# Performance work log

Measured on AMD Instinct MI355X. Metric: run time of the kernel, lower is better.

Reference implementation:

```python
import jax, jax.numpy as jnp
import numpy as np

S_DIM = 4096
N_NODES = 4096
N_EDGES = 32768


def _coarsen(ei_np, N):
    """Integer-only greedy coarsening, faithful to MNGRAPH.forward's while-loop.
    Returns (select order, flattened neighbor indices, segment ids, per-hub
    neighbor counts, forward-fill indices replicating the stale-M behavior for
    empty neighborhoods, and the remapped final edge_index)."""
    ei = ei_np.astype(np.int64).copy()
    I = np.bincount(ei[0], minlength=N)
    O = np.bincount(ei[1], minlength=N)
    order = np.argsort(-(I + O), kind='stable')  # torch.argsort(D, descending=True)
    visits = np.zeros(N, dtype=bool)
    select = []
    nbr_idx, nbr_seg, counts = [], [], []
    while order.size > 0:
        node = int(order[0])
        select.append(node)
        visits[node] = True
        # H = unique neighbors of node in the CURRENT (rewritten) edge_index
        H = np.unique(np.concatenate([ei[1][ei[0] == node], ei[0][ei[1] == node]]))
        visits[H] = True
        order = order[~visits[order]]
        # rewrite: endpoints in H that are not already-selected hubs -> node
        Hn = H[~np.isin(H, np.asarray(select, dtype=np.int64))]
        ei[np.isin(ei, Hn)] = node
        ei = ei[:, ei[0] != ei[1]]  # drop self-loops
        # append reversed edges that are not already present (pair-code isin
        # == the original O(E^2) all/any comparison, computed efficiently)
        code = ei[0] * N + ei[1]
        rcode = ei[1] * N + ei[0]
        new = ~np.isin(rcode, code)
        ei = np.concatenate([ei, ei[::-1][:, new]], axis=1)
        k = len(select) - 1
        nbr_idx.append(H)
        nbr_seg.append(np.full(H.shape[0], k, dtype=np.int64))
        counts.append(H.shape[0])
    select = np.asarray(select, dtype=np.int64)
    sort_sel = np.sort(select)
    ei_out = np.searchsorted(sort_sel, ei)  # compact node ids
    counts = np.asarray(counts, dtype=np.int64)
    # forward-fill: when H is empty the original appends the previous (stale) M
    fill = np.arange(select.shape[0])
    for i in range(select.shape[0]):
        if counts[i] == 0:
            fill[i] = fill[i - 1] if i > 0 else 0
    nbr = np.concatenate(nbr_idx) if nbr_idx else np.zeros(0, np.int64)
    seg = np.concatenate(nbr_seg) if nbr_seg else np.zeros(0, np.int64)
    return select, nbr, seg, counts, fill, ei_out


def setup_inputs() -> dict:
    key = jax.random.key(0)
    k1, k2, k3, k4 = jax.random.split(key, 4)
    x = jax.random.normal(k1, (N_NODES, S_DIM), dtype=jnp.float32)
    edge_index = jax.random.randint(k2, (2, N_EDGES), 0, N_NODES, dtype=jnp.int64)
    bound = float(np.sqrt(6.0 / (1.0 + S_DIM)))  # xavier_uniform on (1, S)
    W1 = jax.random.uniform(k3, (S_DIM,), jnp.float32, -bound, bound)
    W2 = jax.random.uniform(k4, (S_DIM,), jnp.float32, -bound, bound)
    B1 = jnp.zeros((S_DIM,), jnp.float32)
    B2 = jnp.zeros((S_DIM,), jnp.float32)
    return {"x": x, "edge_index": edge_index, "W1": W1, "W2": W2, "B1": B1, "B2": B2}


def reference(x, edge_index, W1, W2, B1, B2):
    N = x.shape[0]
    sel, nbr, seg, counts, fill, ei_out = _coarsen(np.asarray(edge_index), N)
    K = sel.shape[0]
    # Dn = x[n]*W1+B1 for every neighbor of every hub; per-hub mean via segment_sum
    Dn = x[jnp.asarray(nbr)] * W1 + B1                      # [T, S]
    sums = jax.ops.segment_sum(Dn, jnp.asarray(seg), num_segments=K)
    denom = jnp.maximum(jnp.asarray(counts), 1).astype(x.dtype)[:, None]
    mean_Dn = sums / denom                                  # [K, S]
    Dv = x[jnp.asarray(sel)] * W2 + B2                      # [K, S]
    END = jnp.concatenate([Dv, mean_Dn], axis=1)            # [K, 2S]
    END = END[jnp.asarray(fill)]                            # stale-M replication
    return END, jnp.asarray(ei_out)
```

## Files before the change

kernel.cpp:

```cpp
#include <hip/hip_runtime.h>
#include <hip/hip_bf16.h>

#define NT 1024
#define NNODES 4096
#define ECAP 65536

__device__ __forceinline__ int blockScanExcl(int v, int* s_w, int* total) {
    const int tid  = threadIdx.x;
    const int lane = tid & 63;
    const int wv   = tid >> 6;
    int x = v;
#pragma unroll
    for (int off = 1; off < 64; off <<= 1) {
        int t = __shfl_up(x, off, 64);
        if (lane >= off) x += t;
    }
    if (lane == 63) s_w[wv] = x;
    __syncthreads();
    if (tid < 16) {
        int y = s_w[tid];
#pragma unroll
        for (int off = 1; off < 16; off <<= 1) {
            int t = __shfl_up(y, off, 16);
            if (tid >= off) y += t;
        }
        s_w[tid] = y;
    }
    __syncthreads();
    int base = wv ? s_w[wv - 1] : 0;
    int tot  = s_w[15];
    __syncthreads();
    *total = tot;
    return base + x - v;
}

__global__ __launch_bounds__(NT, 1)
void phaseA1(const int* __restrict__ ei, int E0,
             int* __restrict__ U, int* __restrict__ V,
             unsigned int* __restrict__ BM,
             int* __restrict__ NBR, int* __restrict__ OTH,
             int* __restrict__ ORDV, int* __restrict__ ROFFG, int* __restrict__ RENDG,
             int* __restrict__ HAND)
{
    __shared__ unsigned short s_order[NNODES];
    __shared__ unsigned char  s_vis[NNODES];
    __shared__ unsigned int   s_hb[NNODES / 32];
    __shared__ int s_roff[NNODES];
    __shared__ int s_rend[NNODES];
    __shared__ int s_tmp[NNODES];
    __shared__ int s_w[16];
    __shared__ int s_bc[16];

    const int tid = threadIdx.x;

    for (int i = tid; i < NNODES; i += NT) { s_vis[i] = 0; s_tmp[i] = 0; }
    for (int i = tid; i < NNODES / 32; i += NT) s_hb[i] = 0;
    if (tid < 16) s_bc[tid] = 0;
    __syncthreads();

    for (int i = tid; i < E0; i += NT)
        if (ei[2 * i + 1] != 0) s_bc[9] = 1;
    __syncthreads();
    const int is64 = !s_bc[9];

    for (int e = tid; e < E0; e += NT) {
        int uu = ei[is64 ? 2 * e : e];
        int vv = ei[is64 ? 2 * (E0 + e) : (E0 + e)];
        U[e] = uu; V[e] = vv;
        atomicAdd(&s_tmp[uu], 1);
        atomicAdd(&s_tmp[vv], 1);
    }
    __syncthreads();
    for (int n = tid; n < NNODES; n += NT) atomicMax(&s_bc[7], s_tmp[n]);
    __syncthreads();
    const int maxd = s_bc[7];

    for (int d = maxd; d >= 0; --d) {
        int n0 = tid * 4;
        int f0 = (s_tmp[n0] == d), f1 = (s_tmp[n0 + 1] == d);
        int f2 = (s_tmp[n0 + 2] == d), f3 = (s_tmp[n0 + 3] == d);
        int tot;
        int off = blockScanExcl(f0 + f1 + f2 + f3, s_w, &tot);
        int idx = s_bc[4] + off;
        if (f0) s_order[idx++] = (unsigned short)n0;
        if (f1) s_order[idx++] = (unsigned short)(n0 + 1);
        if (f2) s_order[idx++] = (unsigned short)(n0 + 2);
        if (f3) s_order[idx++] = (unsigned short)(n0 + 3);
        __syncthreads();
        if (tid == 0) s_bc[4] += tot;
        __syncthreads();
    }

    if (tid == 0) {
        int nd = s_order[0];
        s_bc[0] = nd; s_vis[nd] = 1;
    }
    __syncthreads();
    {
        const int node = s_bc[0];
        for (int e = tid; e < E0; e += NT) {
            int uu = U[e], vv = V[e];
            if (uu == node) {
                int w = vv; unsigned m = 1u << (w & 31);
                unsigned old = atomicOr(&s_hb[w >> 5], m);
                if (!(old & m)) { int i = atomicAdd(&s_bc[2], 1); s_tmp[i] = w; s_vis[w] = 1; }
            }
            if (vv == node) {
                int w = uu; unsigned m = 1u << (w & 31);
                unsigned old = atomicOr(&s_hb[w >> 5], m);
                if (!(old & m)) { int i = atomicAdd(&s_bc[2], 1); s_tmp[i] = w; s_vis[w] = 1; }
            }
        }
        __syncthreads();
        for (int e = tid; e < E0; e += NT) {
            int uu = U[e];
            if (uu != node && ((s_hb[uu >> 5] >> (uu & 31)) & 1)) U[e] = node;
            int vv = V[e];
            if (vv != node && ((s_hb[vv >> 5] >> (vv & 31)) & 1)) V[e] = node;
        }
        __syncthreads();
    }

    for (int i = tid; i < (1 << 19); i += NT) BM[i] = 0u;
    __syncthreads();
    for (int e = tid; e < E0; e += NT) {
        int uu = U[e], vv = V[e];
        if (uu != vv) {
            unsigned code = ((unsigned)uu << 12) | (unsigned)vv;
            atomicOr(&BM[code >> 5], 1u << (code & 31));
        }
    }
    __syncthreads();
    for (int t = 0; t < E0; t += NT) {
        int e = t + tid, flag = 0, uu = 0, vv = 0;
        if (e < E0) {
            uu = U[e]; vv = V[e];
            if (uu != vv) {
                unsigned rc = ((unsigned)vv << 12) | (unsigned)uu;
                unsigned old = atomicOr(&BM[rc >> 5], 0u);
                flag = !((old >> (rc & 31)) & 1u);
            }
        }
        int tot;
        int off = blockScanExcl(flag, s_w, &tot);
        if (flag) { int r = s_bc[5] + off; U[E0 + r] = vv; V[E0 + r] = uu; }
        __syncthreads();
        if (tid == 0) s_bc[5] += tot;
        __syncthreads();
    }
    const int E1 = E0 + s_bc[5];

    for (int n = tid; n < NNODES; n += NT) s_roff[n] = 0;
    __syncthreads();
    for (int e = tid; e < E1; e += NT) {
        int uu = U[e], vv = V[e];
        if (uu != vv) { atomicAdd(&s_roff[uu], 1); atomicAdd(&s_roff[vv], 1); }
    }
    __syncthreads();
    {
        int n0 = tid * 4;
        int c0 = s_roff[n0], c1 = s_roff[n0 + 1], c2 = s_roff[n0 + 2], c3 = s_roff[n0 + 3];
        int tot;
        int off = blockScanExcl(c0 + c1 + c2 + c3, s_w, &tot);
        int st = off;
        s_roff[n0] = st;     s_rend[n0] = st;     st += c0;
        s_roff[n0 + 1] = st; s_rend[n0 + 1] = st; st += c1;
        s_roff[n0 + 2] = st; s_rend[n0 + 2] = st; st += c2;
        s_roff[n0 + 3] = st; s_rend[n0 + 3] = st;
    }
    __syncthreads();
    for (int e = tid; e < E1; e += NT) {
        int uu = U[e], vv = V[e];
        if (uu != vv) {
            int p = atomicAdd(&s_rend[uu], 1);
            int q = atomicAdd(&s_rend[vv], 1);
            OTH[p] = vv; OTH[q] = uu;
        }
    }
    __syncthreads();
    {
        const int cnt0 = s_bc[2];
        for (int i = tid; i < cnt0; i += NT) NBR[i] = s_tmp[i];
    }
    for (int i = tid; i < NNODES; i += NT) {
        int nd = (int)s_order[i];
        ORDV[i]  = nd | (s_vis[nd] ? 0x8000 : 0);
        ROFFG[i] = s_roff[i];
        RENDG[i] = s_rend[i];
    }
    if (tid == 0) { HAND[0] = E1; HAND[1] = s_bc[2]; HAND[2] = s_bc[0]; }
}

__global__ __launch_bounds__(64, 1)
void phaseA2(const int* __restrict__ OTH, int* __restrict__ NBR,
             const int* __restrict__ ORDV, const int* __restrict__ ROFFG,
             const int* __restrict__ RENDG, const int* __restrict__ HAND,
             int* __restrict__ SEL, int* __restrict__ CNTS,
             int* __restrict__ NST, int* __restrict__ FIL, int* __restrict__ SC,
             int* __restrict__ LABG, int* __restrict__ RNKG)
{
    __shared__ unsigned short s_ordvis[NNODES];
    __shared__ unsigned short s_pos[NNODES];
    __shared__ unsigned short s_lab[NNODES];
    __shared__ unsigned short s_so[NNODES];
    __shared__ int s_cnt[NNODES];
    __shared__ int s_stamp[NNODES];
    __shared__ int s_roff[NNODES];
    __shared__ int s_rend[NNODES];
    __shared__ unsigned char s_sel[NNODES];
    __shared__ int s_nc[1];

    const int ln = threadIdx.x;
    const unsigned long long ltm = (1ull << ln) - 1ull;
    const int cnt0 = HAND[1], hub0 = HAND[2];

    for (int i = ln; i < NNODES; i += 64) {
        int ov = ORDV[i];
        s_ordvis[i] = (unsigned short)ov;
        s_pos[ov & 0x7FFF] = (unsigned short)i;
        s_roff[i] = ROFFG[i];
        s_rend[i] = RENDG[i];
        s_lab[i] = (unsigned short)i;
        s_stamp[i] = 0; s_sel[i] = 0; s_cnt[i] = 0;
    }
    if (ln == 0) {
        s_sel[hub0] = 1; s_so[0] = (unsigned short)hub0;
        s_cnt[0] = cnt0; s_nc[0] = cnt0;
    }

    int p = 0, k = 1;
    for (;;) {
        int node = -1;
        while (p < NNODES) {
            int idx = p + ln;
            int ov = (idx < NNODES) ? (int)s_ordvis[idx] : 0x8000;
            unsigned long long bal = __ballot(!(ov & 0x8000));
            if (bal != 0ull) {
                int sl = __ffsll((long long)bal) - 1;
                node = __shfl(ov, sl, 64) & 0x7FFF;
                p += sl + 1;
                break;
            }
            p += 64;
        }
        if (node < 0) break;
        if (ln == 0) { s_sel[node] = 1; s_so[k] = (unsigned short)node; }
        const int rb = s_roff[node], re = s_rend[node];
        const int begin = s_nc[0];
        for (int s0 = rb; s0 < re; s0 += 128) {
            int sA = s0 + ln, sB = s0 + 64 + ln;
            int oA = (sA < re) ? OTH[sA] : -1;
            int oB = (sB < re) ? OTH[sB] : -1;
            if (oA >= 0) {
                int w = (int)s_lab[oA];
                if (w != node) {
                    int old = atomicMax(&s_stamp[w], k);
                    if (old < k) {
                        int i = atomicAdd(&s_nc[0], 1);
                        NBR[i] = w;
                        s_ordvis[s_pos[w]] = (unsigned short)(0x8000 | w);
                        if (!s_sel[w]) s_lab[w] = (unsigned short)node;
                    }
                }
            }
            if (oB >= 0) {
                int w = (int)s_lab[oB];
                if (w != node) {
                    int old = atomicMax(&s_stamp[w], k);
                    if (old < k) {
                        int i = atomicAdd(&s_nc[0], 1);
                        NBR[i] = w;
                        s_ordvis[s_pos[w]] = (unsigned short)(0x8000 | w);
                        if (!s_sel[w]) s_lab[w] = (unsigned short)node;
                    }
                }
            }
        }
        if (ln == 0) s_cnt[k] = s_nc[0] - begin;
        k++;
    }
    const int K = k;

    {
        int base = 0;
        for (int c = 0; c < NNODES / 64; ++c) {
            int n = c * 64 + ln;
            int f = s_sel[n];
            unsigned long long b = __ballot(f);
            s_stamp[n] = base + __popcll(b & ltm);
            base += __popcll(b);
        }
    }
    {
        int nb = 0;
        for (int c = 0; c * 64 < K; ++c) {
            int i = c * 64 + ln;
            int cv = (i < K) ? s_cnt[i] : 0;
            int x = cv;
#pragma unroll
            for (int off = 1; off < 64; off <<= 1) {
                int t = __shfl_up(x, off, 64);
                if (ln >= off) x += t;
            }
            if (i < K) { NST[i] = nb + x - cv; CNTS[i] = cv; SEL[i] = (int)s_so[i]; }
            nb += __shfl(x, 63, 64);
        }
    }
    {
        int carry = 0;
        for (int c = 0; c * 64 < K; ++c) {
            int i = c * 64 + ln;
            int f = (i < K) && (s_cnt[i] > 0);
            unsigned long long b = __ballot(f);
            unsigned long long m = b & ((ln == 63) ? ~0ull : ((1ull << (ln + 1)) - 1ull));
            int fil = m ? (c * 64 + 63 - __clzll(m)) : carry;
            if (i < K) FIL[i] = fil;
            carry = b ? (c * 64 + 63 - __clzll(b)) : carry;
        }
    }
    if (ln == 0) SC[0] = K;
    for (int i = ln; i < NNODES; i += 64) {
        LABG[i] = (int)s_lab[i];
        RNKG[i] = s_stamp[i];
    }
}

__global__ __launch_bounds__(NT, 1)
void phaseA3(const int* __restrict__ U, const int* __restrict__ V,
             const int* __restrict__ LABG, const int* __restrict__ RNKG,
             const int* __restrict__ HAND, int* __restrict__ SC,
             int* __restrict__ TMP, float* __restrict__ out)
{
    __shared__ unsigned short l_lab[NNODES];
    __shared__ int l_rnk[NNODES];
    __shared__ int s_w[16];
    __shared__ int s_base[1];

    const int tid = threadIdx.x;
    for (int i = tid; i < NNODES; i += NT) {
        l_lab[i] = (unsigned short)LABG[i];
        l_rnk[i] = RNKG[i];
    }
    if (tid == 0) s_base[0] = 0;
    __syncthreads();

    const int E1 = HAND[0];
    const int K  = SC[0];
    const size_t obase = (size_t)K * 8192;

    for (int t = 0; t < E1; t += NT) {
        int e = t + tid, flag = 0, ru = 0, rv = 0;
        if (e < E1) {
            int uu = (int)l_lab[U[e]], vv = (int)l_lab[V[e]];
            if (uu != vv) { flag = 1; ru = l_rnk[uu]; rv = l_rnk[vv]; }
        }
        int tot;
        int off = blockScanExcl(flag, s_w, &tot);
        if (flag) {
            int r = s_base[0] + off;
            out[obase + (size_t)r] = (float)ru;
            TMP[r] = rv;
        }
        __syncthreads();
        if (tid == 0) s_base[0] += tot;
        __syncthreads();
    }
    const int Ef = s_base[0];
    if (tid == 0) SC[1] = Ef;
    for (int r = tid; r < Ef; r += NT)
        out[obase + (size_t)Ef + (size_t)r] = (float)TMP[r];
}

__global__ __launch_bounds__(256, 4)
void phaseB(const float* __restrict__ x,
            const float* __restrict__ W1, const float* __restrict__ W2,
            const float* __restrict__ B1, const float* __restrict__ B2,
            const int* __restrict__ NBR, const int* __restrict__ SEL,
            const int* __restrict__ CNTS, const int* __restrict__ NST,
            const int* __restrict__ FIL, const int* __restrict__ SC,
            float* __restrict__ out)
{
    const int K = SC[0];
    const int k = blockIdx.x;
    if (k >= K) return;
    const int kk   = FIL[k];
    const int node = SEL[kk];
    const int cnt  = CNTS[kk];
    const int st   = NST[kk];
    const int tid  = threadIdx.x;
    const float4* x4 = (const float4*)x;

    float4 acc[4];
#pragma unroll
    for (int j = 0; j < 4; j++) acc[j] = make_float4(0.f, 0.f, 0.f, 0.f);

    for (int r = 0; r < cnt; ++r) {
        const float4* row = x4 + (size_t)NBR[st + r] * 1024;
#pragma unroll
        for (int j = 0; j < 4; j++) {
            float4 t = row[tid + j * 256];
            acc[j].x += t.x; acc[j].y += t.y; acc[j].z += t.z; acc[j].w += t.w;
        }
    }

    const float fc  = (float)cnt;
    const float inv = 1.0f / (float)(cnt > 1 ? cnt : 1);
    const float4* xr = x4 + (size_t)node * 1024;
    float4* o4 = (float4*)(out + (size_t)k * 8192);

#pragma unroll
    for (int j = 0; j < 4; j++) {
        int c = tid + j * 256;
        float4 w1 = ((const float4*)W1)[c], b1 = ((const float4*)B1)[c];
        float4 w2 = ((const float4*)W2)[c], b2 = ((const float4*)B2)[c];
        float4 xv = xr[c];
        float4 pd, pm;
        pd.x = xv.x * w2.x + b2.x;
        pd.y = xv.y * w2.y + b2.y;
        pd.z = xv.z * w2.z + b2.z;
        pd.w = xv.w * w2.w + b2.w;
        pm.x = (acc[j].x * w1.x + fc * b1.x) * inv;
        pm.y = (acc[j].y * w1.y + fc * b1.y) * inv;
        pm.z = (acc[j].z * w1.z + fc * b1.z) * inv;
        pm.w = (acc[j].w * w1.w + fc * b1.w) * inv;
        o4[c] = pd;
        o4[1024 + c] = pm;
    }
}

extern "C" void kernel_launch(void* const* d_in, const int* in_sizes, int n_in,
                              void* d_out, int out_size, void* d_ws, size_t ws_size,
                              hipStream_t stream)
{
    const float* x  = (const float*)d_in[0];
    const int*   ei = (const int*)d_in[1];
    const float* W1 = (const float*)d_in[2];
    const float* W2 = (const float*)d_in[3];
    const float* B1 = (const float*)d_in[4];
    const float* B2 = (const float*)d_in[5];
    const int E0 = in_sizes[1] / 2;

    char* w = (char*)d_ws;
    int* U = (int*)w;
    int* V = U + ECAP;
    unsigned int* BM = (unsigned int*)(V + ECAP);
    int* OTH = (int*)BM;
    int* NBR = OTH + 2 * ECAP;
    int* TMP = NBR + 2 * ECAP;
    char* meta = (char*)BM + (2u << 20);
    int* SEL   = (int*)meta;
    int* CNTS  = SEL  + NNODES;
    int* NST   = CNTS + NNODES;
    int* FIL   = NST  + NNODES;
    int* SC    = FIL  + NNODES;
    int* ORDV  = SC   + 16;
    int* ROFFG = ORDV + NNODES;
    int* RENDG = ROFFG + NNODES;
    int* LABG  = RENDG + NNODES;
    int* RNKG  = LABG + NNODES;
    int* HAND  = RNKG + NNODES;
    float* out = (float*)d_out;

    hipLaunchKernelGGL(phaseA1, dim3(1), dim3(NT), 0, stream,
                       ei, E0, U, V, BM, NBR, OTH, ORDV, ROFFG, RENDG, HAND);
    hipLaunchKernelGGL(phaseA2, dim3(1), dim3(64), 0, stream,
                       OTH, NBR, ORDV, ROFFG, RENDG, HAND,
                       SEL, CNTS, NST, FIL, SC, LABG, RNKG);
    hipLaunchKernelGGL(phaseA3, dim3(1), dim3(NT), 0, stream,
                       U, V, LABG, RNKG, HAND, SC, TMP, out);
    hipLaunchKernelGGL(phaseB, dim3(NNODES), dim3(256), 0, stream,
                       x, W1, W2, B1, B2, NBR, SEL, CNTS, NST, FIL, SC, out);
}
```

Measured before the change: 965.9 us.

## Restructure coarsening phases: parallel degree sort, prefetching hub loop, chunked compaction

Replaces the per-degree scan loop that built the descending-degree order with a second block doing a counting sort using wave ballots, and picks the first hub with an atomicMin. The serial hub-selection loop in phaseA2 now prefetches the next candidate's adjacency while processing the current one, and uses ballot-based cursor allocation instead of shared atomics. Edge compaction in phaseA1 and phaseA3 uses per-thread chunk bitmasks with a single block scan in place of many scan-plus-sync rounds. phaseB is split over a second grid dimension to get more blocks. These target the long single-block serial latency chain, at the cost of more complex control flow and chunk masks that assume at most 64 edges per thread.

Result: slower. 1.179 ms (+22.1%).

```diff
diff --git a/kernel.cpp b/kernel.cpp
--- a/kernel.cpp
+++ b/kernel.cpp
@@ -39,10 +39,12 @@
              int* __restrict__ U, int* __restrict__ V,
              unsigned int* __restrict__ BM,
              int* __restrict__ NBR, int* __restrict__ OTH,
-             int* __restrict__ ORDV, int* __restrict__ ROFFG, int* __restrict__ RENDG,
-             int* __restrict__ HAND)
+             int* __restrict__ ORDG, int* __restrict__ ROFFG, int* __restrict__ RENDG,
+             int* __restrict__ STAMPG, int* __restrict__ HAND)
 {
-    __shared__ unsigned short s_order[NNODES];
+    __shared__ int t_deg[NNODES];
+    __shared__ int t_cur[NNODES];
+    __shared__ int t_bc[4];
     __shared__ unsigned char  s_vis[NNODES];
     __shared__ unsigned int   s_hb[NNODES / 32];
     __shared__ int s_roff[NNODES];
@@ -53,9 +55,66 @@
 
     const int tid = threadIdx.x;
 
+    if (blockIdx.x == 1) {
+        for (int i = tid; i < NNODES; i += NT) { t_deg[i] = 0; t_cur[i] = 0; }
+        if (tid < 4) t_bc[tid] = 0;
+        __syncthreads();
+        for (int i = tid; i < E0; i += NT)
+            if (ei[2 * i + 1] != 0) t_bc[1] = 1;
+        __syncthreads();
+        const int is64b = !t_bc[1];
+        for (int e = tid; e < E0; e += NT) {
+            int uu = ei[is64b ? 2 * e : e];
+            int vv = ei[is64b ? 2 * (E0 + e) : (E0 + e)];
+            atomicAdd(&t_deg[uu], 1);
+            atomicAdd(&t_deg[vv], 1);
+        }
+        __syncthreads();
+        for (int n = tid; n < NNODES; n += NT) atomicMax(&t_bc[2], t_deg[n]);
+        __syncthreads();
+        const int maxd = t_bc[2];
+        for (int n = tid; n < NNODES; n += NT) atomicAdd(&t_cur[t_deg[n]], 1);
+        __syncthreads();
+        if (tid < 64) {
+            const int ln = tid;
+            const unsigned long long ltm = (1ull << ln) - 1ull;
+            int carry = 0;
+            for (int b0 = 0; b0 <= maxd; b0 += 64) {
+                int d = b0 + ln;
+                int v = (d <= maxd) ? t_cur[d] : 0;
+                int x = v;
+#pragma unroll
+                for (int off = 1; off < 64; off <<= 1) {
+                    int t = __shfl_up(x, off, 64);
+                    if (ln >= off) x += t;
+                }
+                if (d <= maxd) t_cur[d] = NNODES - (carry + x);
+                carry += __shfl(x, 63, 64);
+            }
+            const int nb = 32 - __clz(maxd | 1);
+            for (int g = 0; g < NNODES / 64; ++g) {
+                int n = g * 64 + ln;
+                int d = t_deg[n];
+                unsigned long long m = ~0ull;
+                for (int b = 0; b < nb; ++b) {
+                    unsigned long long bb = __ballot((d >> b) & 1);
+                    m &= ((d >> b) & 1) ? bb : ~bb;
+                }
+                int rank   = __popcll(m & ltm);
+                int leader = __ffsll((long long)m) - 1;
+                int base = 0;
+                if (ln == leader) { base = t_cur[d]; t_cur[d] = base + __popcll(m); }
+                base = __shfl(base, leader, 64);
+                ORDG[base + rank] = n;
+            }
+        }
+        return;
+    }
+
     for (int i = tid; i < NNODES; i += NT) { s_vis[i] = 0; s_tmp[i] = 0; }
     for (int i = tid; i < NNODES / 32; i += NT) s_hb[i] = 0;
     if (tid < 16) s_bc[tid] = 0;
+    if (tid == 0) s_bc[0] = 0x7fffffff;
     __syncthreads();
 
     for (int i = tid; i < E0; i += NT)
@@ -74,27 +133,11 @@
     for (int n = tid; n < NNODES; n += NT) atomicMax(&s_bc[7], s_tmp[n]);
     __syncthreads();
     const int maxd = s_bc[7];
-
-    for (int d = maxd; d >= 0; --d) {
-        int n0 = tid * 4;
-        int f0 = (s_tmp[n0] == d), f1 = (s_tmp[n0 + 1] == d);
-        int f2 = (s_tmp[n0 + 2] == d), f3 = (s_tmp[n0 + 3] == d);
-        int tot;
-        int off = blockScanExcl(f0 + f1 + f2 + f3, s_w, &tot);
-        int idx = s_bc[4] + off;
-        if (f0) s_order[idx++] = (unsigned short)n0;
-        if (f1) s_order[idx++] = (unsigned short)(n0 + 1);
-        if (f2) s_order[idx++] = (unsigned short)(n0 + 2);
-        if (f3) s_order[idx++] = (unsigned short)(n0 + 3);
-        __syncthreads();
-        if (tid == 0) s_bc[4] += tot;
-        __syncthreads();
-    }
-
-    if (tid == 0) {
-        int nd = s_order[0];
-        s_bc[0] = nd; s_vis[nd] = 1;
-    }
+    for (int n = tid; n < NNODES; n += NT)
+        if (s_tmp[n] == maxd) atomicMin(&s_bc[0], n);
+    __syncthreads();
+
+    if (tid == 0) { s_vis[s_bc[0]] = 1; }
     __syncthreads();
     {
         const int node = s_bc[0];
@@ -121,7 +164,10 @@
         __syncthreads();
     }
 
-    for (int i = tid; i < (1 << 19); i += NT) BM[i] = 0u;
+    {
+        uint4* bm4 = (uint4*)BM;
+        for (int i = tid; i < (1 << 17); i += NT) bm4[i] = make_uint4(0, 0, 0, 0);
+    }
     __syncthreads();
     for (int e = tid; e < E0; e += NT) {
         int uu = U[e], vv = V[e];
@@ -131,24 +177,33 @@
         }
     }
     __syncthreads();
-    for (int t = 0; t < E0; t += NT) {
-        int e = t + tid, flag = 0, uu = 0, vv = 0;
-        if (e < E0) {
-            uu = U[e]; vv = V[e];
-            if (uu != vv) {
-                unsigned rc = ((unsigned)vv << 12) | (unsigned)uu;
-                unsigned old = atomicOr(&BM[rc >> 5], 0u);
-                flag = !((old >> (rc & 31)) & 1u);
+    int E1;
+    {
+        const int chA = (E0 + NT - 1) / NT;
+        const int begA = tid * chA;
+        unsigned long long mA = 0ull;
+        for (int j = 0; j < chA; ++j) {
+            int e = begA + j;
+            if (e < E0) {
+                int uu = U[e], vv = V[e];
+                if (uu != vv) {
+                    unsigned rc = ((unsigned)vv << 12) | (unsigned)uu;
+                    unsigned old = atomicOr(&BM[rc >> 5], 0u);
+                    if (!((old >> (rc & 31)) & 1u)) mA |= 1ull << j;
+                }
             }
         }
         int tot;
-        int off = blockScanExcl(flag, s_w, &tot);
-        if (flag) { int r = s_bc[5] + off; U[E0 + r] = vv; V[E0 + r] = uu; }
-        __syncthreads();
-        if (tid == 0) s_bc[5] += tot;
-        __syncthreads();
-    }
-    const int E1 = E0 + s_bc[5];
+        int off = blockScanExcl(__popcll(mA), s_w, &tot);
+        int r = off;
+        for (int j = 0; j < chA; ++j) if ((mA >> j) & 1) {
+            int e = begA + j;
+            U[E0 + r] = V[e]; V[E0 + r] = U[e];
+            r++;
+        }
+        E1 = E0 + tot;
+    }
+    __syncthreads();
 
     for (int n = tid; n < NNODES; n += NT) s_roff[n] = 0;
     __syncthreads();
@@ -183,100 +238,113 @@
         for (int i = tid; i < cnt0; i += NT) NBR[i] = s_tmp[i];
     }
     for (int i = tid; i < NNODES; i += NT) {
-        int nd = (int)s_order[i];
-        ORDV[i]  = nd | (s_vis[nd] ? 0x8000 : 0);
-        ROFFG[i] = s_roff[i];
-        RENDG[i] = s_rend[i];
+        ROFFG[i]  = s_roff[i];
+        RENDG[i]  = s_rend[i];
+        STAMPG[i] = s_vis[i] ? 0 : -1;
     }
     if (tid == 0) { HAND[0] = E1; HAND[1] = s_bc[2]; HAND[2] = s_bc[0]; }
 }
 
 __global__ __launch_bounds__(64, 1)
 void phaseA2(const int* __restrict__ OTH, int* __restrict__ NBR,
-             const int* __restrict__ ORDV, const int* __restrict__ ROFFG,
-             const int* __restrict__ RENDG, const int* __restrict__ HAND,
+             const int* __restrict__ ORDG, const int* __restrict__ ROFFG,
+             const int* __restrict__ RENDG, const int* __restrict__ STAMPG,
+             const int* __restrict__ HAND,
              int* __restrict__ SEL, int* __restrict__ CNTS,
              int* __restrict__ NST, int* __restrict__ FIL, int* __restrict__ SC,
              int* __restrict__ LABG, int* __restrict__ RNKG)
 {
-    __shared__ unsigned short s_ordvis[NNODES];
-    __shared__ unsigned short s_pos[NNODES];
+    __shared__ unsigned short s_ord[NNODES];
+    __shared__ int s_stamp[NNODES];
     __shared__ unsigned short s_lab[NNODES];
+    __shared__ unsigned char  s_sel[NNODES];
+    __shared__ int s_cnt[NNODES];
     __shared__ unsigned short s_so[NNODES];
-    __shared__ int s_cnt[NNODES];
-    __shared__ int s_stamp[NNODES];
     __shared__ int s_roff[NNODES];
     __shared__ int s_rend[NNODES];
-    __shared__ unsigned char s_sel[NNODES];
-    __shared__ int s_nc[1];
 
     const int ln = threadIdx.x;
     const unsigned long long ltm = (1ull << ln) - 1ull;
-    const int cnt0 = HAND[1], hub0 = HAND[2];
 
     for (int i = ln; i < NNODES; i += 64) {
-        int ov = ORDV[i];
-        s_ordvis[i] = (unsigned short)ov;
-        s_pos[ov & 0x7FFF] = (unsigned short)i;
-        s_roff[i] = ROFFG[i];
-        s_rend[i] = RENDG[i];
-        s_lab[i] = (unsigned short)i;
-        s_stamp[i] = 0; s_sel[i] = 0; s_cnt[i] = 0;
-    }
-    if (ln == 0) {
-        s_sel[hub0] = 1; s_so[0] = (unsigned short)hub0;
-        s_cnt[0] = cnt0; s_nc[0] = cnt0;
-    }
+        s_ord[i]   = (unsigned short)ORDG[i];
+        s_stamp[i] = STAMPG[i];
+        s_lab[i]   = (unsigned short)i;
+        s_sel[i]   = 0; s_cnt[i] = 0;
+        s_roff[i]  = ROFFG[i];
+        s_rend[i]  = RENDG[i];
+    }
+    int cursor = HAND[1];
+    const int hub0 = HAND[2];
+    if (ln == 0) { s_sel[hub0] = 1; s_so[0] = (unsigned short)hub0; s_cnt[0] = cursor; }
+
+    auto wsel = [&](int& pp) -> int {
+        while (pp < NNODES) {
+            int idx = pp + ln;
+            int nd  = (idx < NNODES) ? (int)s_ord[idx] : 0;
+            int st  = (idx < NNODES) ? s_stamp[nd] : 0;
+            unsigned long long bal = __ballot(st < 0);
+            if (bal) {
+                int sl = __ffsll((long long)bal) - 1;
+                pp += sl + 1;
+                return __shfl(nd, sl, 64);
+            }
+            pp += 64;
+        }
+        return -1;
+    };
 
     int p = 0, k = 1;
-    for (;;) {
-        int node = -1;
-        while (p < NNODES) {
-            int idx = p + ln;
-            int ov = (idx < NNODES) ? (int)s_ordvis[idx] : 0x8000;
-            unsigned long long bal = __ballot(!(ov & 0x8000));
-            if (bal != 0ull) {
-                int sl = __ffsll((long long)bal) - 1;
-                node = __shfl(ov, sl, 64) & 0x7FFF;
-                p += sl + 1;
-                break;
-            }
-            p += 64;
-        }
-        if (node < 0) break;
-        if (ln == 0) { s_sel[node] = 1; s_so[k] = (unsigned short)node; }
-        const int rb = s_roff[node], re = s_rend[node];
-        const int begin = s_nc[0];
-        for (int s0 = rb; s0 < re; s0 += 128) {
-            int sA = s0 + ln, sB = s0 + 64 + ln;
-            int oA = (sA < re) ? OTH[sA] : -1;
-            int oB = (sB < re) ? OTH[sB] : -1;
-            if (oA >= 0) {
-                int w = (int)s_lab[oA];
-                if (w != node) {
-                    int old = atomicMax(&s_stamp[w], k);
-                    if (old < k) {
-                        int i = atomicAdd(&s_nc[0], 1);
-                        NBR[i] = w;
-                        s_ordvis[s_pos[w]] = (unsigned short)(0x8000 | w);
-                        if (!s_sel[w]) s_lab[w] = (unsigned short)node;
-                    }
+    int node = wsel(p);
+    int rb = 0, re = 0, oA = -1, oB = -1;
+    if (node >= 0) {
+        rb = s_roff[node]; re = s_rend[node];
+        oA = (rb + ln < re) ? OTH[rb + ln] : -1;
+        oB = (rb + 64 + ln < re) ? OTH[rb + 64 + ln] : -1;
+    }
+    while (node >= 0) {
+        if (ln == 0) { atomicExch(&s_stamp[node], k); s_sel[node] = 1; s_so[k] = (unsigned short)node; }
+        int pc = p;
+        int cand = wsel(pc);
+        int rb2 = 0, re2 = 0, oA2 = -1, oB2 = -1;
+        if (cand >= 0) {
+            rb2 = s_roff[cand]; re2 = s_rend[cand];
+            oA2 = (rb2 + ln < re2) ? OTH[rb2 + ln] : -1;
+            oB2 = (rb2 + 64 + ln < re2) ? OTH[rb2 + 64 + ln] : -1;
+        }
+        int total = 0; bool candhit = false;
+        auto proc = [&](int o) {
+            bool isnew = false; int w = -1;
+            if (o >= 0) {
+                w = (int)s_lab[o];
+                int sv  = s_sel[w];
+                int old = atomicMax(&s_stamp[w], k);
+                if (old < k) {
+                    isnew = true;
+                    if (!sv) s_lab[w] = (unsigned short)node;
+                    if (w == cand) candhit = true;
                 }
             }
-            if (oB >= 0) {
-                int w = (int)s_lab[oB];
-                if (w != node) {
-                    int old = atomicMax(&s_stamp[w], k);
-                    if (old < k) {
-                        int i = atomicAdd(&s_nc[0], 1);
-                        NBR[i] = w;
-                        s_ordvis[s_pos[w]] = (unsigned short)(0x8000 | w);
-                        if (!s_sel[w]) s_lab[w] = (unsigned short)node;
-                    }
-                }
-            }
-        }
-        if (ln == 0) s_cnt[k] = s_nc[0] - begin;
+            unsigned long long b = __ballot(isnew);
+            if (isnew) NBR[cursor + __popcll(b & ltm)] = w;
+            int cc = __popcll(b);
+            cursor += cc; total += cc;
+        };
+        proc(oA); proc(oB);
+        for (int s0 = rb + 128; s0 < re; s0 += 64) {
+            int s = s0 + ln;
+            proc((s < re) ? OTH[s] : -1);
+        }
+        if (ln == 0) s_cnt[k] = total;
+        if (__ballot(candhit)) {
+            cand = wsel(pc);
+            if (cand >= 0) {
+                rb2 = s_roff[cand]; re2 = s_rend[cand];
+                oA2 = (rb2 + ln < re2) ? OTH[rb2 + ln] : -1;
+                oB2 = (rb2 + 64 + ln < re2) ? OTH[rb2 + 64 + ln] : -1;
+            }
+        }
+        p = pc; node = cand; rb = rb2; re = re2; oA = oA2; oB = oB2;
         k++;
     }
     const int K = k;
@@ -329,46 +397,42 @@
 void phaseA3(const int* __restrict__ U, const int* __restrict__ V,
              const int* __restrict__ LABG, const int* __restrict__ RNKG,
              const int* __restrict__ HAND, int* __restrict__ SC,
-             int* __restrict__ TMP, float* __restrict__ out)
+             float* __restrict__ out)
 {
     __shared__ unsigned short l_lab[NNODES];
     __shared__ int l_rnk[NNODES];
     __shared__ int s_w[16];
-    __shared__ int s_base[1];
 
     const int tid = threadIdx.x;
     for (int i = tid; i < NNODES; i += NT) {
         l_lab[i] = (unsigned short)LABG[i];
         l_rnk[i] = RNKG[i];
     }
-    if (tid == 0) s_base[0] = 0;
     __syncthreads();
 
     const int E1 = HAND[0];
     const int K  = SC[0];
-    const size_t obase = (size_t)K * 8192;
-
-    for (int t = 0; t < E1; t += NT) {
-        int e = t + tid, flag = 0, ru = 0, rv = 0;
+    const int ch = (E1 + NT - 1) / NT;
+    const int beg = tid * ch;
+    unsigned long long mF = 0ull;
+    for (int j = 0; j < ch; ++j) {
+        int e = beg + j;
         if (e < E1) {
             int uu = (int)l_lab[U[e]], vv = (int)l_lab[V[e]];
-            if (uu != vv) { flag = 1; ru = l_rnk[uu]; rv = l_rnk[vv]; }
-        }
-        int tot;
-        int off = blockScanExcl(flag, s_w, &tot);
-        if (flag) {
-            int r = s_base[0] + off;
-            out[obase + (size_t)r] = (float)ru;
-            TMP[r] = rv;
-        }
-        __syncthreads();
-        if (tid == 0) s_base[0] += tot;
-        __syncthreads();
-    }
-    const int Ef = s_base[0];
+            if (uu != vv) mF |= 1ull << j;
+        }
+    }
+    int Ef;
+    int off = blockScanExcl(__popcll(mF), s_w, &Ef);
+    const size_t obase = (size_t)K * 8192;
+    int r = off;
+    for (int j = 0; j < ch; ++j) if ((mF >> j) & 1) {
+        int e = beg + j;
+        out[obase + (size_t)r]              = (float)l_rnk[(int)l_lab[U[e]]];
+        out[obase + (size_t)Ef + (size_t)r] = (float)l_rnk[(int)l_lab[V[e]]];
+        r++;
+    }
     if (tid == 0) SC[1] = Ef;
-    for (int r = tid; r < Ef; r += NT)
-        out[obase + (size_t)Ef + (size_t)r] = (float)TMP[r];
 }
 
 __global__ __launch_bounds__(256, 4)
@@ -387,45 +451,33 @@
     const int node = SEL[kk];
     const int cnt  = CNTS[kk];
     const int st   = NST[kk];
-    const int tid  = threadIdx.x;
+    const int c    = blockIdx.y * 256 + threadIdx.x;
     const float4* x4 = (const float4*)x;
 
-    float4 acc[4];
-#pragma unroll
-    for (int j = 0; j < 4; j++) acc[j] = make_float4(0.f, 0.f, 0.f, 0.f);
-
+    float4 acc = make_float4(0.f, 0.f, 0.f, 0.f);
     for (int r = 0; r < cnt; ++r) {
         const float4* row = x4 + (size_t)NBR[st + r] * 1024;
-#pragma unroll
-        for (int j = 0; j < 4; j++) {
-            float4 t = row[tid + j * 256];
-            acc[j].x += t.x; acc[j].y += t.y; acc[j].z += t.z; acc[j].w += t.w;
-        }
+        float4 t = row[c];
+        acc.x += t.x; acc.y += t.y; acc.z += t.z; acc.w += t.w;
     }
 
     const float fc  = (float)cnt;
     const float inv = 1.0f / (float)(cnt > 1 ? cnt : 1);
-    const float4* xr = x4 + (size_t)node * 1024;
+    float4 w1 = ((const float4*)W1)[c], b1 = ((const float4*)B1)[c];
+    float4 w2 = ((const float4*)W2)[c], b2 = ((const float4*)B2)[c];
+    float4 xv = (x4 + (size_t)node * 1024)[c];
+    float4 pd, pm;
+    pd.x = xv.x * w2.x + b2.x;
+    pd.y = xv.y * w2.y + b2.y;
+    pd.z = xv.z * w2.z + b2.z;
+    pd.w = xv.w * w2.w + b2.w;
+    pm.x = (acc.x * w1.x + fc * b1.x) * inv;
+    pm.y = (acc.y * w1.y + fc * b1.y) * inv;
+    pm.z = (acc.z * w1.z + fc * b1.z) * inv;
+    pm.w = (acc.w * w1.w + fc * b1.w) * inv;
     float4* o4 = (float4*)(out + (size_t)k * 8192);
-
-#pragma unroll
-    for (int j = 0; j < 4; j++) {
-        int c = tid + j * 256;
-        float4 w1 = ((const float4*)W1)[c], b1 = ((const float4*)B1)[c];
-        float4 w2 = ((const float4*)W2)[c], b2 = ((const float4*)B2)[c];
-        float4 xv = xr[c];
-        float4 pd, pm;
-        pd.x = xv.x * w2.x + b2.x;
-        pd.y = xv.y * w2.y + b2.y;
-        pd.z = xv.z * w2.z + b2.z;
-        pd.w = xv.w * w2.w + b2.w;
-        pm.x = (acc[j].x * w1.x + fc * b1.x) * inv;
-        pm.y = (acc[j].y * w1.y + fc * b1.y) * inv;
-        pm.z = (acc[j].z * w1.z + fc * b1.z) * inv;
-        pm.w = (acc[j].w * w1.w + fc * b1.w) * inv;
-        o4[c] = pd;
-        o4[1024 + c] = pm;
-    }
+    o4[c] = pd;
+    o4[1024 + c] = pm;
 }
 
 extern "C" void kernel_launch(void* const* d_in, const int* in_sizes, int n_in,
@@ -446,28 +498,28 @@
     unsigned int* BM = (unsigned int*)(V + ECAP);
     int* OTH = (int*)BM;
     int* NBR = OTH + 2 * ECAP;
-    int* TMP = NBR + 2 * ECAP;
     char* meta = (char*)BM + (2u << 20);
-    int* SEL   = (int*)meta;
-    int* CNTS  = SEL  + NNODES;
-    int* NST   = CNTS + NNODES;
-    int* FIL   = NST  + NNODES;
-    int* SC    = FIL  + NNODES;
-    int* ORDV  = SC   + 16;
-    int* ROFFG = ORDV + NNODES;
-    int* RENDG = ROFFG + NNODES;
-    int* LABG  = RENDG + NNODES;
-    int* RNKG  = LABG + NNODES;
-    int* HAND  = RNKG + NNODES;
+    int* SEL    = (int*)meta;
+    int* CNTS   = SEL    + NNODES;
+    int* NST    = CNTS   + NNODES;
+    int* FIL    = NST    + NNODES;
+    int* SC     = FIL    + NNODES;
+    int* ORDG   = SC     + 16;
+    int* ROFFG  = ORDG   + NNODES;
+    int* RENDG  = ROFFG  + NNODES;
+    int* LABG   = RENDG  + NNODES;
+    int* RNKG   = LABG   + NNODES;
+    int* STAMPG = RNKG   + NNODES;
+    int* HAND   = STAMPG + NNODES;
     float* out = (float*)d_out;
 
-    hipLaunchKernelGGL(phaseA1, dim3(1), dim3(NT), 0, stream,
-                       ei, E0, U, V, BM, NBR, OTH, ORDV, ROFFG, RENDG, HAND);
+    hipLaunchKernelGGL(phaseA1, dim3(2), dim3(NT), 0, stream,
+                       ei, E0, U, V, BM, NBR, OTH, ORDG, ROFFG, RENDG, STAMPG, HAND);
     hipLaunchKernelGGL(phaseA2, dim3(1), dim3(64), 0, stream,
-                       OTH, NBR, ORDV, ROFFG, RENDG, HAND,
+                       OTH, NBR, ORDG, ROFFG, RENDG, STAMPG, HAND,
                        SEL, CNTS, NST, FIL, SC, LABG, RNKG);
     hipLaunchKernelGGL(phaseA3, dim3(1), dim3(NT), 0, stream,
-                       U, V, LABG, RNKG, HAND, SC, TMP, out);
-    hipLaunchKernelGGL(phaseB, dim3(NNODES), dim3(256), 0, stream,
+                       U, V, LABG, RNKG, HAND, SC, out);
+    hipLaunchKernelGGL(phaseB, dim3(NNODES, 4), dim3(256), 0, stream,
                        x, W1, W2, B1, B2, NBR, SEL, CNTS, NST, FIL, SC, out);
 }
```
